# Optimization experiments

Hardware: AMD Instinct MI355X
Metric: run time of the kernel (lower is better)

## Reference

```python
import jax, jax.numpy as jnp
import numpy as np


def setup_inputs() -> dict:
    key = jax.random.key(0)
    ks = jax.random.split(key, 5)
    B, H, W, C = 8, 64, 64, 64
    Cfg = C // 8
    x = jax.random.normal(ks[0], (B, H, W, C), dtype=jnp.float32)
    # glorot-ish scale for 1x1 conv kernels
    kernel_f = jax.random.normal(ks[1], (1, 1, C, Cfg), dtype=jnp.float32) * (1.0 / np.sqrt(C))
    kernel_g = jax.random.normal(ks[2], (1, 1, C, Cfg), dtype=jnp.float32) * (1.0 / np.sqrt(C))
    kernel_h = jax.random.normal(ks[3], (1, 1, C, C), dtype=jnp.float32) * (1.0 / np.sqrt(C))
    bias_f = jnp.zeros((Cfg,), dtype=jnp.float32)
    bias_g = jnp.zeros((Cfg,), dtype=jnp.float32)
    bias_h = jnp.zeros((C,), dtype=jnp.float32)
    gamma = jax.random.uniform(ks[4], (1,), dtype=jnp.float32)
    return {"x": x, "kernel_f": kernel_f, "kernel_g": kernel_g, "kernel_h": kernel_h,
            "bias_f": bias_f, "bias_g": bias_g, "bias_h": bias_h, "gamma": gamma}


def reference(x, kernel_f, kernel_g, kernel_h, bias_f, bias_g, bias_h, gamma):
    B, H, W, C = x.shape
    N = H * W
    xf = x.reshape(B, N, C)  # hw_flatten; 1x1 conv == per-pixel matmul over channels
    f = xf @ kernel_f.reshape(C, -1) + bias_f          # [B, N, C//8]
    g = xf @ kernel_g.reshape(C, -1) + bias_g          # [B, N, C//8]
    h = xf @ kernel_h.reshape(C, -1) + bias_h          # [B, N, C]
    s = jnp.einsum('bnd,bmd->bnm', g, f)               # [B, N, N] = g @ f^T
    beta = jax.nn.softmax(s, axis=-1)
    o = jnp.einsum('bnm,bmc->bnc', beta, h)            # [B, N, C]
    out = gamma * o + xf
    return out.reshape(B, H, W, C)
```

## Files before the change

### kernel.cpp

```cpp
#include <hip/hip_runtime.h>

typedef _Float16 f16;
typedef _Float16 f16x8 __attribute__((ext_vector_type(8)));
typedef short s16x8 __attribute__((ext_vector_type(8)));
typedef float f32x4 __attribute__((ext_vector_type(4)));
typedef float f32x16 __attribute__((ext_vector_type(16)));
typedef unsigned int u32x4 __attribute__((ext_vector_type(4)));

#define SM_OFF_NAT 11.0903548889f
#define MFMA32F16(a, b, c) __builtin_amdgcn_mfma_f32_32x32x16_f16(a, b, c, 0, 0, 0)
#define MFMA32BF16(a, b, c) __builtin_amdgcn_mfma_f32_32x32x16_bf16(a, b, c, 0, 0, 0)

typedef __attribute__((address_space(1))) const unsigned int* gas_t;
typedef __attribute__((address_space(3))) unsigned int* las_t;

static __device__ inline void gload16(const void* g, void* l) {
    __builtin_amdgcn_global_load_lds((gas_t)g, (las_t)l, 16, 0, 0);
}

static __device__ inline void perm32swap(unsigned int& a, unsigned int& b) {
    asm("v_permlane32_swap_b32 %0, %1" : "+v"(a), "+v"(b));
}

static __device__ inline unsigned int cvt_pk_bf16(float a, float b) {
    unsigned int r;
    asm("v_cvt_pk_bf16_f32 %0, %1, %2" : "=v"(r) : "v"(a), "v"(b));
    return r;
}

static __device__ inline unsigned int pack_bf16_pair(float a, float b) {
    unsigned int ua = __builtin_bit_cast(unsigned int, a) + 0x8000u;
    unsigned int ub = __builtin_bit_cast(unsigned int, b) + 0x8000u;
    return __builtin_amdgcn_perm(ub, ua, 0x07060302u);
}

static __device__ inline unsigned short f2bf(float f) {
    unsigned int u = __builtin_bit_cast(unsigned int, f);
    u += 0x7FFFu + ((u >> 16) & 1u);
    return (unsigned short)(u >> 16);
}

__global__ __launch_bounds__(256) void proj_kernel(
    const float* __restrict__ x, const float* __restrict__ Kf,
    const float* __restrict__ Kg, const float* __restrict__ Kh,
    const float* __restrict__ bf, const float* __restrict__ bg,
    const float* __restrict__ bh,
    f16* __restrict__ fO, f16* __restrict__ gO, unsigned short* __restrict__ hF)
{
    __shared__ float KT[80 * 64];
    __shared__ float bias[80];
    const int tid = threadIdx.x;

    for (int i = tid; i < 512; i += 256) {
        int d = i >> 3, j = i & 7;
        KT[j * 64 + d] = Kf[i];
        KT[(8 + j) * 64 + d] = Kg[i];
    }
    for (int i = tid; i < 4096; i += 256) {
        int d = i >> 6, c = i & 63;
        KT[(16 + c) * 64 + d] = Kh[i];
    }
    if (tid < 8) { bias[tid] = bf[tid]; bias[8 + tid] = bg[tid]; }
    if (tid >= 16 && tid < 80) bias[tid] = bh[tid - 16];
    __syncthreads();

    const int quarter = tid >> 6;
    const int px = blockIdx.x * 64 + (tid & 63);
    const float4* xp = (const float4*)(x + (size_t)px * 64);
    float4 xr[16];
#pragma unroll
    for (int i = 0; i < 16; ++i) xr[i] = xp[i];

    float res[20];
    const int c0 = quarter * 20;
#pragma unroll
    for (int cc = 0; cc < 20; ++cc) {
        const int c = c0 + cc;
        float acc = bias[c];
        const float4* wv = (const float4*)(KT + c * 64);
#pragma unroll
        for (int i = 0; i < 16; ++i) {
            float4 w = wv[i];
            acc = fmaf(xr[i].x, w.x, acc);
            acc = fmaf(xr[i].y, w.y, acc);
            acc = fmaf(xr[i].z, w.z, acc);
            acc = fmaf(xr[i].w, w.w, acc);
        }
        res[cc] = acc;
    }

    const int b = px >> 12, n = px & 4095;
    const size_t hbase = (size_t)b * 262144 + (size_t)(n >> 4) * 1024
                       + (size_t)((n >> 3) & 1) * 256 + (n & 7);
    if (quarter == 0) {
        f16x8 fv, gv, fpad, gpad;
#pragma unroll
        for (int j = 0; j < 8; ++j) {
            fv[j] = (f16)res[j]; gv[j] = (f16)res[8 + j];
            fpad[j] = (f16)0.f;  gpad[j] = (f16)0.f;
        }
        fpad[0] = (f16)1.f;
        gpad[0] = (f16)(-SM_OFF_NAT);
        *(f16x8*)(fO + (size_t)px * 16)     = fv;
        *(f16x8*)(fO + (size_t)px * 16 + 8) = fpad;
        *(f16x8*)(gO + (size_t)px * 16)     = gv;
        *(f16x8*)(gO + (size_t)px * 16 + 8) = gpad;
#pragma unroll
        for (int cc = 16; cc < 20; ++cc) {
            const int hc = c0 + cc - 16;
            hF[hbase + (hc >> 5) * 512 + (hc & 31) * 8] = f2bf(res[cc]);
        }
    } else {
#pragma unroll
        for (int cc = 0; cc < 20; ++cc) {
            const int hc = c0 + cc - 16;
            hF[hbase + (hc >> 5) * 512 + (hc & 31) * 8] = f2bf(res[cc]);
        }
    }
}

template<int NSPLIT>
__global__ __launch_bounds__(256, 4) void attn15_kernel(
    const f16* __restrict__ fO, const f16* __restrict__ gO,
    const unsigned short* __restrict__ hF, const float* __restrict__ x,
    const float* __restrict__ gamma, float* __restrict__ out,
    unsigned short* __restrict__ po, float* __restrict__ pml)
{
    __shared__ __align__(16) char lds[2][8192];

    const int tid  = threadIdx.x;
    const int w    = tid >> 6;
    const int lane = tid & 63;
    const int q5   = lane & 31;
    const int hi   = lane >> 5;

    const int b = blockIdx.x & 7;
    int kc, qt;
    if (NSPLIT == 8)      { kc = (blockIdx.x >> 3) & 7; qt = blockIdx.x >> 6; }
    else if (NSPLIT == 4) { kc = (blockIdx.x >> 3) & 3; qt = blockIdx.x >> 5; }
    else if (NSPLIT == 2) { kc = (blockIdx.x >> 3) & 1; qt = blockIdx.x >> 4; }
    else                  { kc = 0;                     qt = blockIdx.x >> 3; }

    const int KEYS = 4096 / NSPLIT;
    const int NIT  = KEYS / 64;
    const int k0   = kc * KEYS;
    const int qrow = qt * 128 + w * 32 + q5;

    const char* hTile = (const char*)hF + ((size_t)b * 262144 + (size_t)k0 * 64) * 2;
    const f16*  fbase = fO + ((size_t)b * 4096 + k0) * 16;

    const f16x8 gfrag = *(const f16x8*)(gO + ((size_t)b * 4096 + qrow) * 16 + hi * 8);

    f32x16 acc0, acc1;
#pragma unroll
    for (int i = 0; i < 16; ++i) { acc0[i] = 0.f; acc1[i] = 0.f; }
    float lpart = 0.f;

#define STAGE_H(KT_, BI_) do {                                                  \
        const char* hg_ = hTile + (size_t)(KT_) * 8192 + w * 2048 + (size_t)lane * 16; \
        char* hl_ = &lds[BI_][0] + w * 2048;                                    \
        gload16(hg_, hl_);                                                      \
        gload16(hg_ + 1024, hl_ + 1024);                                        \
    } while (0)

    STAGE_H(0, 0);
    f16x8 faA = *(const f16x8*)(fbase + (size_t)q5 * 16 + hi * 8);
    f16x8 faB = *(const f16x8*)(fbase + (size_t)(32 + q5) * 16 + hi * 8);
    __syncthreads();

    for (int t = 0; t < NIT; ++t) {
        const int cur = t & 1;
        if (t + 1 < NIT) STAGE_H(t + 1, cur ^ 1);

        const f16x8 fa0 = faA, fa1 = faB;
        if (t + 1 < NIT) {
            const f16* fp = fbase + (size_t)((t + 1) * 64 + q5) * 16 + hi * 8;
            faA = *(const f16x8*)(fp);
            faB = *(const f16x8*)(fp + 512);
        }

        f32x16 zc;
#pragma unroll
        for (int i = 0; i < 16; ++i) zc[i] = 0.f;
        f32x16 s0 = MFMA32F16(fa0, gfrag, zc);
        f32x16 s1 = MFMA32F16(fa1, gfrag, zc);

#pragma unroll
        for (int i = 0; i < 16; ++i) {
            s0[i] = __expf(s0[i]);
            s1[i] = __expf(s1[i]);
        }

        {
            float ls[16];
#pragma unroll
            for (int i = 0; i < 16; ++i) ls[i] = s0[i] + s1[i];
#pragma unroll
            for (int st = 8; st >= 1; st >>= 1)
#pragma unroll
                for (int i = 0; i < st; ++i) ls[i] += ls[i + st];
            lpart += ls[0];
        }

        unsigned int wr[16];
#pragma unroll
        for (int i = 0; i < 8; ++i) {
            wr[i]     = pack_bf16_pair(s0[2 * i], s0[2 * i + 1]);
            wr[8 + i] = pack_bf16_pair(s1[2 * i], s1[2 * i + 1]);
        }

        perm32swap(wr[0], wr[2]);   perm32swap(wr[1], wr[3]);
        perm32swap(wr[4], wr[6]);   perm32swap(wr[5], wr[7]);
        perm32swap(wr[8], wr[10]);  perm32swap(wr[9], wr[11]);
        perm32swap(wr[12], wr[14]); perm32swap(wr[13], wr[15]);

        const unsigned short* hl = (const unsigned short*)&lds[cur][0];
#pragma unroll
        for (int kk = 0; kk < 4; ++kk) {
            u32x4 tv;
            tv[0] = wr[kk * 4 + 0]; tv[1] = wr[kk * 4 + 1];
            tv[2] = wr[kk * 4 + 2]; tv[3] = wr[kk * 4 + 3];
            const s16x8 pf = __builtin_bit_cast(s16x8, tv);
            const s16x8 ha0 = *(const s16x8*)(hl + kk * 1024 + lane * 8);
            const s16x8 ha1 = *(const s16x8*)(hl + kk * 1024 + 512 + lane * 8);
            acc0 = MFMA32BF16(ha0, pf, acc0);
            acc1 = MFMA32BF16(ha1, pf, acc1);
        }

        if (t + 1 < NIT) __syncthreads();
    }
#undef STAGE_H

    lpart += __shfl_xor(lpart, 32);

    if (NSPLIT == 1) {
        const float rin = 1.f / lpart;
        const float gm = gamma[0];
        const size_t qg = (size_t)b * 4096 + qrow;
#pragma unroll
        for (int cb = 0; cb < 2; ++cb)
#pragma unroll
            for (int r = 0; r < 4; ++r) {
                const size_t o = qg * 64 + cb * 32 + r * 8 + hi * 4;
                f32x4 v;
#pragma unroll
                for (int j = 0; j < 4; ++j) {
                    const float a = (cb == 0) ? acc0[4 * r + j] : acc1[4 * r + j];
                    v[j] = fmaf(gm, a * rin, x[o + j]);
                }
                *(f32x4*)(out + o) = v;
            }
    } else {
        unsigned short* pob = po + (size_t)((kc * 8 + b) * 128 + qt * 4 + w) * 2048;
#pragma unroll
        for (int cb = 0; cb < 2; ++cb)
#pragma unroll
            for (int r = 0; r < 4; ++r) {
                uint2 v;
                const float a0 = (cb == 0) ? acc0[4 * r + 0] : acc1[4 * r + 0];
                const float a1 = (cb == 0) ? acc0[4 * r + 1] : acc1[4 * r + 1];
                const float a2 = (cb == 0) ? acc0[4 * r + 2] : acc1[4 * r + 2];
                const float a3 = (cb == 0) ? acc0[4 * r + 3] : acc1[4 * r + 3];
                v.x = cvt_pk_bf16(a0, a1);
                v.y = cvt_pk_bf16(a2, a3);
                *(uint2*)(pob + (cb * 4 + r) * 256 + lane * 4) = v;
            }
        if (lane < 32)
            pml[(size_t)(kc * 8 + b) * 4096 + qrow] = lpart;
    }
}

template<int NS>
__global__ __launch_bounds__(256) void combine_kernel(
    const unsigned short* __restrict__ po, const float* __restrict__ pml,
    const float* __restrict__ x, const float* __restrict__ gamma,
    float* __restrict__ out)
{
    const int t    = blockIdx.x * 256 + threadIdx.x;
    const int lane = t & 63;
    const int r    = (t >> 6) & 3;
    const int cb   = (t >> 8) & 1;
    const int w    = (t >> 9) & 3;
    const int qt   = (t >> 11) & 31;
    const int b    = (t >> 16) & 7;
    const int q    = qt * 128 + w * 32 + (lane & 31);
    const int c    = cb * 32 + r * 8 + (lane >> 5) * 4;

    float denom = 0.f;
    f32x4 num;
#pragma unroll
    for (int j = 0; j < 4; ++j) num[j] = 0.f;
#pragma unroll
    for (int kc = 0; kc < NS; ++kc) {
        denom += pml[(size_t)(kc * 8 + b) * 4096 + q];
        const uint2 v = *(const uint2*)(po + (size_t)((kc * 8 + b) * 128 + qt * 4 + w) * 2048
                                           + (cb * 4 + r) * 256 + lane * 4);
        num[0] += __builtin_bit_cast(float, v.x << 16);
        num[1] += __builtin_bit_cast(float, v.x & 0xFFFF0000u);
        num[2] += __builtin_bit_cast(float, v.y << 16);
        num[3] += __builtin_bit_cast(float, v.y & 0xFFFF0000u);
    }
    const float sc = gamma[0] / denom;
    const size_t o = ((size_t)b * 4096 + q) * 64 + c;
    const f32x4 xv = *(const f32x4*)(x + o);
    f32x4 ov;
#pragma unroll
    for (int j = 0; j < 4; ++j) ov[j] = fmaf(sc, num[j], xv[j]);
    *(f32x4*)(out + o) = ov;
}

extern "C" void kernel_launch(void* const* d_in, const int* in_sizes, int n_in,
                              void* d_out, int out_size, void* d_ws, size_t ws_size,
                              hipStream_t stream) {
    const float* x     = (const float*)d_in[0];
    const float* Kf    = (const float*)d_in[1];
    const float* Kg    = (const float*)d_in[2];
    const float* Kh    = (const float*)d_in[3];
    const float* bf    = (const float*)d_in[4];
    const float* bg    = (const float*)d_in[5];
    const float* bh    = (const float*)d_in[6];
    const float* gamma = (const float*)d_in[7];
    float* out = (float*)d_out;

    f16* fO = (f16*)d_ws;
    f16* gO = (f16*)((char*)d_ws + (1 << 20));
    unsigned short* hF = (unsigned short*)((char*)d_ws + (2 << 20));
    unsigned short* po = (unsigned short*)((char*)d_ws + (6 << 20));

    const size_t need4 = ((size_t)6 << 20) + ((size_t)16 << 20) + ((size_t)1 << 20);
    const size_t need2 = ((size_t)6 << 20) + ((size_t)8 << 20) + ((size_t)1 << 19);

    hipLaunchKernelGGL(proj_kernel, dim3(512), dim3(256), 0, stream,
                       x, Kf, Kg, Kh, bf, bg, bh, fO, gO, hF);
    if (ws_size >= need4) {
        float* pml = (float*)((char*)d_ws + (22u << 20));
        hipLaunchKernelGGL((attn15_kernel<4>), dim3(1024), dim3(256), 0, stream,
                           fO, gO, hF, x, gamma, out, po, pml);
        hipLaunchKernelGGL((combine_kernel<4>), dim3(2048), dim3(256), 0, stream,
                           po, pml, x, gamma, out);
    } else if (ws_size >= need2) {
        float* pml = (float*)((char*)d_ws + (14u << 20));
        hipLaunchKernelGGL((attn15_kernel<2>), dim3(512), dim3(256), 0, stream,
                           fO, gO, hF, x, gamma, out, po, pml);
        hipLaunchKernelGGL((combine_kernel<2>), dim3(2048), dim3(256), 0, stream,
                           po, pml, x, gamma, out);
    } else {
        hipLaunchKernelGGL((attn15_kernel<1>), dim3(256), dim3(256), 0, stream,
                           fO, gO, hF, x, gamma, out, po, (float*)po);
    }
}
```

Baseline: 67.30 us.

## Compute 1x1 projections with f16 MFMA using a pre-transposed weight kernel

Replaces the scalar FP32 FMA projection kernel with a small prep kernel and an MFMA-based projection. The prep kernel converts the weights to a transposed, padded f16 layout and folds the softmax-offset padding constants into a bias vector. The projection kernel then runs 32x32x16 f16 MFMAs per wave on x converted to f16. This removes the per-block LDS weight staging and the scalar FMA work, at the cost of an extra launch and lower input precision (x and weights rounded to f16 before the matmul).

```diff
diff --git a/kernel.cpp b/kernel.cpp
--- a/kernel.cpp
+++ b/kernel.cpp
@@ -1,6 +1,7 @@
 #include <hip/hip_runtime.h>
 
 typedef _Float16 f16;
+typedef _Float16 f16x2v __attribute__((ext_vector_type(2)));
 typedef _Float16 f16x8 __attribute__((ext_vector_type(8)));
 typedef short s16x8 __attribute__((ext_vector_type(8)));
 typedef float f32x4 __attribute__((ext_vector_type(4)));
@@ -40,87 +41,104 @@
     return (unsigned short)(u >> 16);
 }
 
-__global__ __launch_bounds__(256) void proj_kernel(
-    const float* __restrict__ x, const float* __restrict__ Kf,
-    const float* __restrict__ Kg, const float* __restrict__ Kh,
-    const float* __restrict__ bf, const float* __restrict__ bg,
-    const float* __restrict__ bh,
+__global__ __launch_bounds__(256) void prep_kernel(
+    const float* __restrict__ Kf, const float* __restrict__ Kg,
+    const float* __restrict__ Kh, const float* __restrict__ bf,
+    const float* __restrict__ bg, const float* __restrict__ bh,
+    f16* __restrict__ Wt16, float* __restrict__ biasG)
+{
+    const int tid = blockIdx.x * 256 + threadIdx.x;
+    if (tid < 6144) {
+        const int c = tid >> 6, d = tid & 63;
+        float v = 0.f;
+        if (c < 16)      { if (c < 8)       v = Kf[d * 8 + c]; }
+        else if (c < 32) { if (c - 16 < 8)  v = Kg[d * 8 + (c - 16)]; }
+        else             v = Kh[d * 64 + (c - 32)];
+        Wt16[tid] = (f16)v;
+    }
+    if (tid < 96) {
+        float bv;
+        if (tid < 8)        bv = bf[tid];
+        else if (tid == 8)  bv = 1.0f;
+        else if (tid < 16)  bv = 0.f;
+        else if (tid < 24)  bv = bg[tid - 16];
+        else if (tid == 24) bv = -SM_OFF_NAT;
+        else if (tid < 32)  bv = 0.f;
+        else                bv = bh[tid - 32];
+        biasG[tid] = bv;
+    }
+}
+
+__global__ __launch_bounds__(256) void projm_kernel(
+    const float* __restrict__ x, const f16* __restrict__ Wt16,
+    const float* __restrict__ biasG,
     f16* __restrict__ fO, f16* __restrict__ gO, unsigned short* __restrict__ hF)
 {
-    __shared__ float KT[80 * 64];
-    __shared__ float bias[80];
-    const int tid = threadIdx.x;
-
-    for (int i = tid; i < 512; i += 256) {
-        int d = i >> 3, j = i & 7;
-        KT[j * 64 + d] = Kf[i];
-        KT[(8 + j) * 64 + d] = Kg[i];
-    }
-    for (int i = tid; i < 4096; i += 256) {
-        int d = i >> 6, c = i & 63;
-        KT[(16 + c) * 64 + d] = Kh[i];
-    }
-    if (tid < 8) { bias[tid] = bf[tid]; bias[8 + tid] = bg[tid]; }
-    if (tid >= 16 && tid < 80) bias[tid] = bh[tid - 16];
-    __syncthreads();
-
-    const int quarter = tid >> 6;
-    const int px = blockIdx.x * 64 + (tid & 63);
-    const float4* xp = (const float4*)(x + (size_t)px * 64);
-    float4 xr[16];
-#pragma unroll
-    for (int i = 0; i < 16; ++i) xr[i] = xp[i];
-
-    float res[20];
-    const int c0 = quarter * 20;
-#pragma unroll
-    for (int cc = 0; cc < 20; ++cc) {
-        const int c = c0 + cc;
-        float acc = bias[c];
-        const float4* wv = (const float4*)(KT + c * 64);
-#pragma unroll
-        for (int i = 0; i < 16; ++i) {
-            float4 w = wv[i];
-            acc = fmaf(xr[i].x, w.x, acc);
-            acc = fmaf(xr[i].y, w.y, acc);
-            acc = fmaf(xr[i].z, w.z, acc);
-            acc = fmaf(xr[i].w, w.w, acc);
-        }
-        res[cc] = acc;
-    }
-
-    const int b = px >> 12, n = px & 4095;
-    const size_t hbase = (size_t)b * 262144 + (size_t)(n >> 4) * 1024
-                       + (size_t)((n >> 3) & 1) * 256 + (n & 7);
-    if (quarter == 0) {
-        f16x8 fv, gv, fpad, gpad;
-#pragma unroll
-        for (int j = 0; j < 8; ++j) {
-            fv[j] = (f16)res[j]; gv[j] = (f16)res[8 + j];
-            fpad[j] = (f16)0.f;  gpad[j] = (f16)0.f;
-        }
-        fpad[0] = (f16)1.f;
-        gpad[0] = (f16)(-SM_OFF_NAT);
-        *(f16x8*)(fO + (size_t)px * 16)     = fv;
-        *(f16x8*)(fO + (size_t)px * 16 + 8) = fpad;
-        *(f16x8*)(gO + (size_t)px * 16)     = gv;
-        *(f16x8*)(gO + (size_t)px * 16 + 8) = gpad;
-#pragma unroll
-        for (int cc = 16; cc < 20; ++cc) {
-            const int hc = c0 + cc - 16;
-            hF[hbase + (hc >> 5) * 512 + (hc & 31) * 8] = f2bf(res[cc]);
-        }
-    } else {
-#pragma unroll
-        for (int cc = 0; cc < 20; ++cc) {
-            const int hc = c0 + cc - 16;
-            hF[hbase + (hc >> 5) * 512 + (hc & 31) * 8] = f2bf(res[cc]);
+    const int tid  = threadIdx.x;
+    const int w    = tid >> 6;
+    const int lane = tid & 63;
+    const int c    = lane & 31;
+    const int hi   = lane >> 5;
+
+    const int pxb = (blockIdx.x * 4 + w) * 32;
+    const int px  = pxb + c;
+
+    f16x8 xa[4];
+#pragma unroll
+    for (int ks = 0; ks < 4; ++ks) {
+        const float4* p = (const float4*)(x + (size_t)px * 64 + ks * 16 + hi * 8);
+        const float4 a = p[0], bq = p[1];
+        u32x4 u;
+        u[0] = __builtin_bit_cast(unsigned int, __builtin_amdgcn_cvt_pkrtz(a.x, a.y));
+        u[1] = __builtin_bit_cast(unsigned int, __builtin_amdgcn_cvt_pkrtz(a.z, a.w));
+        u[2] = __builtin_bit_cast(unsigned int, __builtin_amdgcn_cvt_pkrtz(bq.x, bq.y));
+        u[3] = __builtin_bit_cast(unsigned int, __builtin_amdgcn_cvt_pkrtz(bq.z, bq.w));
+        xa[ks] = __builtin_bit_cast(f16x8, u);
+    }
+
+    f32x16 acc0, acc1, acc2;
+#pragma unroll
+    for (int i = 0; i < 16; ++i) { acc0[i] = 0.f; acc1[i] = 0.f; acc2[i] = 0.f; }
+#pragma unroll
+    for (int ks = 0; ks < 4; ++ks) {
+        const f16* wb = Wt16 + (size_t)ks * 16 + hi * 8 + (size_t)c * 64;
+        const f16x8 w0 = *(const f16x8*)(wb);
+        const f16x8 w1 = *(const f16x8*)(wb + 32 * 64);
+        const f16x8 w2 = *(const f16x8*)(wb + 64 * 64);
+        acc0 = MFMA32F16(xa[ks], w0, acc0);
+        acc1 = MFMA32F16(xa[ks], w1, acc1);
+        acc2 = MFMA32F16(xa[ks], w2, acc2);
+    }
+
+    const float b0 = biasG[c], b1 = biasG[32 + c], b2 = biasG[64 + c];
+
+    f16* base0 = (c < 16) ? (fO + c) : (gO + (c - 16));
+#pragma unroll
+    for (int r = 0; r < 16; ++r) {
+        const int prow = (r & 3) + 8 * (r >> 2) + 4 * hi;
+        base0[(size_t)(pxb + prow) * 16] = (f16)(acc0[r] + b0);
+    }
+
+    const int bb = pxb >> 12;
+    const size_t hb0 = (size_t)bb * 262144;
+#pragma unroll
+    for (int t = 0; t < 2; ++t) {
+        const int hc = t * 32 + c;
+        const size_t hchunk = (size_t)(hc >> 5) * 512 + (size_t)(hc & 31) * 8;
+        const float bt = (t == 0) ? b1 : b2;
+#pragma unroll
+        for (int r = 0; r < 16; ++r) {
+            const int prow = (r & 3) + 8 * (r >> 2) + 4 * hi;
+            const int n = (pxb & 4095) + prow;
+            const float v = ((t == 0) ? acc1[r] : acc2[r]) + bt;
+            hF[hb0 + (size_t)(n >> 4) * 1024 + (size_t)((n >> 3) & 1) * 256
+               + hchunk + (n & 7)] = f2bf(v);
         }
     }
 }
 
 template<int NSPLIT>
-__global__ __launch_bounds__(256, 4) void attn15_kernel(
+__global__ __launch_bounds__(256, 4) void attn17_kernel(
     const f16* __restrict__ fO, const f16* __restrict__ gO,
     const unsigned short* __restrict__ hF, const float* __restrict__ x,
     const float* __restrict__ gamma, float* __restrict__ out,
@@ -327,25 +345,41 @@
     unsigned short* hF = (unsigned short*)((char*)d_ws + (2 << 20));
     unsigned short* po = (unsigned short*)((char*)d_ws + (6 << 20));
 
-    const size_t need4 = ((size_t)6 << 20) + ((size_t)16 << 20) + ((size_t)1 << 20);
-    const size_t need2 = ((size_t)6 << 20) + ((size_t)8 << 20) + ((size_t)1 << 19);
-
-    hipLaunchKernelGGL(proj_kernel, dim3(512), dim3(256), 0, stream,
-                       x, Kf, Kg, Kh, bf, bg, bh, fO, gO, hF);
+    const size_t need4 = ((size_t)23 << 20) + (1 << 16);
+    const size_t need2 = ((size_t)14 << 20) + ((size_t)1 << 19) + (1 << 16);
+
     if (ws_size >= need4) {
-        float* pml = (float*)((char*)d_ws + (22u << 20));
-        hipLaunchKernelGGL((attn15_kernel<4>), dim3(1024), dim3(256), 0, stream,
+        float* pml   = (float*)((char*)d_ws + (22u << 20));
+        f16*   Wt16  = (f16*)((char*)d_ws + (23u << 20));
+        float* biasG = (float*)((char*)d_ws + (23u << 20) + 16384);
+        hipLaunchKernelGGL(prep_kernel, dim3(24), dim3(256), 0, stream,
+                           Kf, Kg, Kh, bf, bg, bh, Wt16, biasG);
+        hipLaunchKernelGGL(projm_kernel, dim3(256), dim3(256), 0, stream,
+                           x, Wt16, biasG, fO, gO, hF);
+        hipLaunchKernelGGL((attn17_kernel<4>), dim3(1024), dim3(256), 0, stream,
                            fO, gO, hF, x, gamma, out, po, pml);
         hipLaunchKernelGGL((combine_kernel<4>), dim3(2048), dim3(256), 0, stream,
                            po, pml, x, gamma, out);
     } else if (ws_size >= need2) {
-        float* pml = (float*)((char*)d_ws + (14u << 20));
-        hipLaunchKernelGGL((attn15_kernel<2>), dim3(512), dim3(256), 0, stream,
+        float* pml   = (float*)((char*)d_ws + (14u << 20));
+        f16*   Wt16  = (f16*)((char*)d_ws + (14u << 20) + (1 << 19));
+        float* biasG = (float*)((char*)d_ws + (14u << 20) + (1 << 19) + 16384);
+        hipLaunchKernelGGL(prep_kernel, dim3(24), dim3(256), 0, stream,
+                           Kf, Kg, Kh, bf, bg, bh, Wt16, biasG);
+        hipLaunchKernelGGL(projm_kernel, dim3(256), dim3(256), 0, stream,
+                           x, Wt16, biasG, fO, gO, hF);
+        hipLaunchKernelGGL((attn17_kernel<2>), dim3(512), dim3(256), 0, stream,
                            fO, gO, hF, x, gamma, out, po, pml);
         hipLaunchKernelGGL((combine_kernel<2>), dim3(2048), dim3(256), 0, stream,
                            po, pml, x, gamma, out);
     } else {
-        hipLaunchKernelGGL((attn15_kernel<1>), dim3(256), dim3(256), 0, stream,
+        f16*   Wt16  = (f16*)((char*)d_ws + (6u << 20));
+        float* biasG = (float*)((char*)d_ws + (6u << 20) + 16384);
+        hipLaunchKernelGGL(prep_kernel, dim3(24), dim3(256), 0, stream,
+                           Kf, Kg, Kh, bf, bg, bh, Wt16, biasG);
+        hipLaunchKernelGGL(projm_kernel, dim3(256), dim3(256), 0, stream,
+                           x, Wt16, biasG, fO, gO, hF);
+        hipLaunchKernelGGL((attn17_kernel<1>), dim3(256), dim3(256), 0, stream,
                            fO, gO, hF, x, gamma, out, po, (float*)po);
     }
 }
```

After: 57.49 us. 14.6% less time.
